# Performance work log

Measured on AMD Instinct MI355X. Metric: run time of the kernel, lower is better.

## Reference

```python
import jax, jax.numpy as jnp
import numpy as np

N_NODES = 100000
N_EDGES = 1600000
F_IN = 16
F_OUT = 16
N_BASIS = 4  # per spatial dim; basisTerms = [4, 4]


def linear_basis(u, n):
    """Piecewise-linear (hat) basis, n terms on [-1, 1]. u: [E] -> [E, n]."""
    centers = jnp.linspace(-1.0, 1.0, n, dtype=u.dtype)
    dx = 2.0 / (n - 1)
    return jnp.maximum(0.0, 1.0 - jnp.abs(u[:, None] - centers[None, :]) / dx)


def setup_inputs() -> dict:
    key = jax.random.key(0)
    k1, k2, k3, k4, k5 = jax.random.split(key, 5)
    x = jax.random.normal(k1, (N_NODES, F_IN), dtype=jnp.float32)
    edge_index = jax.random.randint(k2, (2, N_EDGES), 0, N_NODES, dtype=jnp.int64)
    # relative positions normalized to [-1, 1]^2 (as in initializeWeights2D)
    edge_attr = jax.random.uniform(k3, (N_EDGES, 2), dtype=jnp.float32,
                                   minval=-1.0, maxval=1.0)
    # weight: [*basisTerms, inputFeatures, outputFeatures], uniform(-0.05, 0.05)
    weight = jax.random.uniform(k4, (N_BASIS, N_BASIS, F_IN, F_OUT),
                                dtype=jnp.float32, minval=-0.05, maxval=0.05)
    return {"x": x, "edge_index": edge_index, "edge_attr": edge_attr,
            "weight": weight}


def reference(x, edge_index, edge_attr, weight):
    """BasisConvLayer forward, mode='conv', linear basis, no bias/activations.

    For each edge e=(i<-j): msg_e = sum_{u,v} b_u(dx) b_v(dy) * (x_j @ W[u,v]);
    out[i] = sum over incoming edges of msg_e.
    """
    row, col = edge_index[0], edge_index[1]
    x_j = x[col]                                   # [E, F_in] gather
    bx = linear_basis(edge_attr[:, 0], N_BASIS)    # [E, nB]
    by = linear_basis(edge_attr[:, 1], N_BASIS)    # [E, nB]
    # outer product of 1D bases -> [E, nB*nB] interpolation coefficients
    t = (bx[:, :, None] * by[:, None, :]).reshape(-1, N_BASIS * N_BASIS)
    w_flat = weight.reshape(N_BASIS * N_BASIS, F_IN, F_OUT)
    # accumulate over the small fixed basis-term set to avoid [E, Fin, Fout]
    msg = jnp.zeros((x_j.shape[0], F_OUT), dtype=x.dtype)
    for k in range(N_BASIS * N_BASIS):
        msg = msg + t[:, k, None] * (x_j @ w_flat[k])
    out = jax.ops.segment_sum(msg, row, num_segments=N_NODES)  # scatter-add
    return out
```

## Files before the change

### kernel.cpp

```cpp
#include <hip/hip_runtime.h>

#define N_NODES 100000
#define N_EDGES 1600000
#define F 16
#define EDGES_PER_BLOCK 256
#define FSLAB 260

#define OUT_FLOAT4 ((N_NODES * F) / 4)

__global__ __launch_bounds__(256) void zero_out_kernel(float4* __restrict__ out) {
    int i = blockIdx.x * 256 + threadIdx.x;
    if (i < OUT_FLOAT4) out[i] = make_float4(0.f, 0.f, 0.f, 0.f);
}

__global__ __launch_bounds__(256) void basis_conv_edges(
    const float* __restrict__ x,
    const int*   __restrict__ edge_index,
    const float* __restrict__ edge_attr,
    const float* __restrict__ weight,
    float*       __restrict__ out)
{
    __shared__ float wl[F * FSLAB];
    for (int idx = threadIdx.x; idx < 4096; idx += 256) {
        const int f = idx & 15;
        const int i = (idx >> 4) & 15;
        const int k = idx >> 8;
        wl[f * FSLAB + k * 16 + i] = weight[idx];
    }
    __syncthreads();

    const int f = threadIdx.x & 15;
    const int s = threadIdx.x >> 4;
    const int ebase = blockIdx.x * EDGES_PER_BLOCK;

#pragma unroll 1
    for (int it = 0; it < EDGES_PER_BLOCK / 16; ++it) {
        const int e = ebase + it * 16 + s;

        const int row = edge_index[e];
        const int col = edge_index[N_EDGES + e];
        const float2 attr = ((const float2*)edge_attr)[e];

        float fu = (attr.x + 1.0f) * 1.5f;
        int iu = (int)fu; iu = iu < 0 ? 0 : (iu > 2 ? 2 : iu);
        const float wu1 = fu - (float)iu;
        const float wu0 = 1.0f - wu1;

        float fv = (attr.y + 1.0f) * 1.5f;
        int iv = (int)fv; iv = iv < 0 ? 0 : (iv > 2 ? 2 : iv);
        const float wv1 = fv - (float)iv;
        const float wv0 = 1.0f - wv1;

        const int k0 = iu * 4 + iv;
        int   kb[4];
        float tw[4];
        kb[0] = k0;     tw[0] = wu0 * wv0;
        kb[1] = k0 + 1; tw[1] = wu0 * wv1;
        kb[2] = k0 + 4; tw[2] = wu1 * wv0;
        kb[3] = k0 + 5; tw[3] = wu1 * wv1;

        const float4* xv = (const float4*)(x + (size_t)col * 16);
        float xs[16];
#pragma unroll
        for (int q = 0; q < 4; ++q) {
            float4 t4 = xv[q];
            xs[4 * q + 0] = t4.x; xs[4 * q + 1] = t4.y;
            xs[4 * q + 2] = t4.z; xs[4 * q + 3] = t4.w;
        }

        float msg = 0.0f;
#pragma unroll
        for (int p = 0; p < 4; ++p) {
            const float t = tw[p];
            const float4* wp = (const float4*)&wl[f * FSLAB + kb[p] * 16];
#pragma unroll
            for (int i4 = 0; i4 < 4; ++i4) {
                const float4 w = wp[i4];
                msg += t * (xs[4 * i4 + 0] * w.x + xs[4 * i4 + 1] * w.y +
                            xs[4 * i4 + 2] * w.z + xs[4 * i4 + 3] * w.w);
            }
        }

        unsafeAtomicAdd(out + (size_t)row * 16 + f, msg);
    }
}

extern "C" void kernel_launch(void* const* d_in, const int* in_sizes, int n_in,
                              void* d_out, int out_size, void* d_ws, size_t ws_size,
                              hipStream_t stream) {
    const float* x  = (const float*)d_in[0];
    const int*   ei = (const int*)d_in[1];
    const float* ea = (const float*)d_in[2];
    const float* w  = (const float*)d_in[3];
    float* out = (float*)d_out;
    (void)out_size; (void)d_ws; (void)ws_size; (void)in_sizes; (void)n_in;

    zero_out_kernel<<<(OUT_FLOAT4 + 255) / 256, 256, 0, stream>>>((float4*)out);

    const int blocks = N_EDGES / EDGES_PER_BLOCK;
    basis_conv_edges<<<blocks, 256, 0, stream>>>(x, ei, ea, w, out);
}
```

Baseline: 179.0 us.

## Compute edge messages with bf16 MFMA over dense basis-weighted features

```diff
diff --git a/kernel.cpp b/kernel.cpp
--- a/kernel.cpp
+++ b/kernel.cpp
@@ -3,85 +3,107 @@
 #define N_NODES 100000
 #define N_EDGES 1600000
 #define F 16
-#define EDGES_PER_BLOCK 256
-#define FSLAB 260
+
+#define EDGES_PER_BLOCK 512
+#define GROUPS_PER_WAVE 8
 
 #define OUT_FLOAT4 ((N_NODES * F) / 4)
+
+typedef __attribute__((ext_vector_type(8))) short bf16x8;
+typedef __attribute__((ext_vector_type(4))) float f32x4;
 
 __global__ __launch_bounds__(256) void zero_out_kernel(float4* __restrict__ out) {
     int i = blockIdx.x * 256 + threadIdx.x;
     if (i < OUT_FLOAT4) out[i] = make_float4(0.f, 0.f, 0.f, 0.f);
 }
 
-__global__ __launch_bounds__(256) void basis_conv_edges(
+__device__ __forceinline__ unsigned pk_bf16(float lo, float hi) {
+    unsigned r;
+    asm("v_cvt_pk_bf16_f32 %0, %1, %2" : "=v"(r) : "v"(lo), "v"(hi));
+    return r;
+}
+
+__global__ __launch_bounds__(256) void basis_conv_mfma(
     const float* __restrict__ x,
     const int*   __restrict__ edge_index,
     const float* __restrict__ edge_attr,
     const float* __restrict__ weight,
     float*       __restrict__ out)
 {
-    __shared__ float wl[F * FSLAB];
-    for (int idx = threadIdx.x; idx < 4096; idx += 256) {
-        const int f = idx & 15;
-        const int i = (idx >> 4) & 15;
-        const int k = idx >> 8;
-        wl[f * FSLAB + k * 16 + i] = weight[idx];
+    const int lane = threadIdx.x & 63;
+    const int wid  = threadIdx.x >> 6;
+    const int e15  = lane & 15;
+    const int fo   = lane & 15;
+    const int c    = lane >> 4;
+    const int hv   = c >> 1;
+    const int i0   = (c & 1) * 8;
+
+    bf16x8 bw[8];
+#pragma unroll
+    for (int m = 0; m < 8; ++m) {
+        const float* wp = weight + (2 * m + hv) * 256 + i0 * 16 + fo;
+        union { bf16x8 v; unsigned u[4]; } bb;
+#pragma unroll
+        for (int p = 0; p < 4; ++p)
+            bb.u[p] = pk_bf16(wp[(2 * p) * 16], wp[(2 * p + 1) * 16]);
+        bw[m] = bb.v;
     }
-    __syncthreads();
 
-    const int f = threadIdx.x & 15;
-    const int s = threadIdx.x >> 4;
-    const int ebase = blockIdx.x * EDGES_PER_BLOCK;
+    const int wbase = blockIdx.x * EDGES_PER_BLOCK + wid * (16 * GROUPS_PER_WAVE);
 
 #pragma unroll 1
-    for (int it = 0; it < EDGES_PER_BLOCK / 16; ++it) {
-        const int e = ebase + it * 16 + s;
+    for (int g = 0; g < GROUPS_PER_WAVE; ++g) {
+        const int eg = wbase + g * 16;
 
-        const int row = edge_index[e];
-        const int col = edge_index[N_EDGES + e];
-        const float2 attr = ((const float2*)edge_attr)[e];
+        const int col   = edge_index[N_EDGES + eg + e15];
+        const float2 at = ((const float2*)edge_attr)[eg + e15];
 
-        float fu = (attr.x + 1.0f) * 1.5f;
+        float fu = (at.x + 1.0f) * 1.5f;
         int iu = (int)fu; iu = iu < 0 ? 0 : (iu > 2 ? 2 : iu);
-        const float wu1 = fu - (float)iu;
-        const float wu0 = 1.0f - wu1;
+        const float wu1 = fu - (float)iu, wu0 = 1.0f - wu1;
+        float fv = (at.y + 1.0f) * 1.5f;
+        int iv = (int)fv; iv = iv < 0 ? 0 : (iv > 2 ? 2 : iv);
+        const float wv1 = fv - (float)iv, wv0 = 1.0f - wv1;
 
-        float fv = (attr.y + 1.0f) * 1.5f;
-        int iv = (int)fv; iv = iv < 0 ? 0 : (iv > 2 ? 2 : iv);
-        const float wv1 = fv - (float)iv;
-        const float wv0 = 1.0f - wv1;
+        const float bu0 = iu == 0 ? wu0 : 0.f;
+        const float bu1 = iu == 0 ? wu1 : (iu == 1 ? wu0 : 0.f);
+        const float bu2 = iu == 2 ? wu0 : (iu == 1 ? wu1 : 0.f);
+        const float bu3 = iu == 2 ? wu1 : 0.f;
+        const float bv0 = iv == 0 ? wv0 : 0.f;
+        const float bv1 = iv == 0 ? wv1 : (iv == 1 ? wv0 : 0.f);
+        const float bv2 = iv == 2 ? wv0 : (iv == 1 ? wv1 : 0.f);
+        const float bv3 = iv == 2 ? wv1 : 0.f;
 
-        const int k0 = iu * 4 + iv;
-        int   kb[4];
-        float tw[4];
-        kb[0] = k0;     tw[0] = wu0 * wv0;
-        kb[1] = k0 + 1; tw[1] = wu0 * wv1;
-        kb[2] = k0 + 4; tw[2] = wu1 * wv0;
-        kb[3] = k0 + 5; tw[3] = wu1 * wv1;
+        const float bvE = hv ? bv1 : bv0;
+        const float bvO = hv ? bv3 : bv2;
 
-        const float4* xv = (const float4*)(x + (size_t)col * 16);
-        float xs[16];
+        const float4* xv = (const float4*)(x + (size_t)col * 16 + i0);
+        const float4 xa = xv[0], xb = xv[1];
+
+        f32x4 acc0 = {0.f, 0.f, 0.f, 0.f};
+        f32x4 acc1 = {0.f, 0.f, 0.f, 0.f};
 #pragma unroll
-        for (int q = 0; q < 4; ++q) {
-            float4 t4 = xv[q];
-            xs[4 * q + 0] = t4.x; xs[4 * q + 1] = t4.y;
-            xs[4 * q + 2] = t4.z; xs[4 * q + 3] = t4.w;
+        for (int m = 0; m < 8; ++m) {
+            const float bu = (m >> 1) == 0 ? bu0 : (m >> 1) == 1 ? bu1
+                           : (m >> 1) == 2 ? bu2 : bu3;
+            const float t = bu * ((m & 1) ? bvO : bvE);
+            union { bf16x8 v; unsigned u[4]; } aa;
+            aa.u[0] = pk_bf16(t * xa.x, t * xa.y);
+            aa.u[1] = pk_bf16(t * xa.z, t * xa.w);
+            aa.u[2] = pk_bf16(t * xb.x, t * xb.y);
+            aa.u[3] = pk_bf16(t * xb.z, t * xb.w);
+            if (m & 1)
+                acc1 = __builtin_amdgcn_mfma_f32_16x16x32_bf16(aa.v, bw[m], acc1, 0, 0, 0);
+            else
+                acc0 = __builtin_amdgcn_mfma_f32_16x16x32_bf16(aa.v, bw[m], acc0, 0, 0, 0);
         }
+        const f32x4 acc = acc0 + acc1;
 
-        float msg = 0.0f;
-#pragma unroll
-        for (int p = 0; p < 4; ++p) {
-            const float t = tw[p];
-            const float4* wp = (const float4*)&wl[f * FSLAB + kb[p] * 16];
-#pragma unroll
-            for (int i4 = 0; i4 < 4; ++i4) {
-                const float4 w = wp[i4];
-                msg += t * (xs[4 * i4 + 0] * w.x + xs[4 * i4 + 1] * w.y +
-                            xs[4 * i4 + 2] * w.z + xs[4 * i4 + 3] * w.w);
-            }
-        }
-
-        unsafeAtomicAdd(out + (size_t)row * 16 + f, msg);
+        const int4 r4 = *(const int4*)(edge_index + eg + 4 * c);
+        unsafeAtomicAdd(out + (size_t)r4.x * 16 + fo, acc.x);
+        unsafeAtomicAdd(out + (size_t)r4.y * 16 + fo, acc.y);
+        unsafeAtomicAdd(out + (size_t)r4.z * 16 + fo, acc.z);
+        unsafeAtomicAdd(out + (size_t)r4.w * 16 + fo, acc.w);
     }
 }
 
@@ -98,5 +120,5 @@
     zero_out_kernel<<<(OUT_FLOAT4 + 255) / 256, 256, 0, stream>>>((float4*)out);
 
     const int blocks = N_EDGES / EDGES_PER_BLOCK;
-    basis_conv_edges<<<blocks, 256, 0, stream>>>(x, ei, ea, w, out);
+    basis_conv_mfma<<<blocks, 256, 0, stream>>>(x, ei, ea, w, out);
 }
```

Measured after the change: 165.6 us. -7.5%, faster.
